# Optimization experiments

Measured on AMD Instinct MI355X. Metric: run time of the kernel, lower is better.

The kernel has to match this reference:

```python
import jax, jax.numpy as jnp
import numpy as np

N, E, NG = 4096, 8192, 256
AF, BF, H, L = 9, 4, 128, 3
LN_EPS = 1e-5


def _layernorm(x, g, b):
    mu = jnp.mean(x, axis=-1, keepdims=True)
    var = jnp.var(x, axis=-1, keepdims=True)
    return (x - mu) * jax.lax.rsqrt(var + LN_EPS) * g + b


def setup_inputs() -> dict:
    key = jax.random.key(0)
    ks = jax.random.split(key, 20)
    x = jax.random.normal(ks[0], (N, AF), dtype=jnp.float32)
    edge_index = jax.random.randint(ks[1], (2, E), 0, N, dtype=jnp.int64)
    edge_attr = jax.random.normal(ks[2], (E, BF), dtype=jnp.float32)
    batch = jnp.sort(jax.random.randint(ks[3], (N,), 0, NG, dtype=jnp.int64))
    s = lambda f: 1.0 / np.sqrt(f)
    return {
        "x": x, "edge_index": edge_index, "edge_attr": edge_attr, "batch": batch,
        "atom_w": jax.random.normal(ks[4], (AF, H), jnp.float32) * s(AF),
        "atom_b": jnp.zeros((H,), jnp.float32),
        # per-layer edge-network params, stacked over L layers
        "e1_w": jax.random.normal(ks[5], (L, BF, H), jnp.float32) * s(BF),
        "e1_b": jnp.zeros((L, H), jnp.float32),
        "e2_w": jax.random.normal(ks[6], (L, H, H * H), jnp.float32) * s(H),
        "e2_b": jnp.zeros((L, H * H), jnp.float32),
        "root_w": jax.random.normal(ks[7], (L, H, H), jnp.float32) * s(H),
        "conv_b": jnp.zeros((L, H), jnp.float32),
        "ln_g": jnp.ones((L, H), jnp.float32),
        "ln_b": jnp.zeros((L, H), jnp.float32),
        "head_w1": jax.random.normal(ks[8], (H, H // 2), jnp.float32) * s(H),
        "head_b1": jnp.zeros((H // 2,), jnp.float32),
        "head_w2": jax.random.normal(ks[9], (H // 2, 1), jnp.float32) * s(H // 2),
        "head_b2": jnp.zeros((1,), jnp.float32),
    }


def reference(x, edge_index, edge_attr, batch, atom_w, atom_b, e1_w, e1_b,
              e2_w, e2_b, root_w, conv_b, ln_g, ln_b, head_w1, head_b1,
              head_w2, head_b2):
    src, dst = edge_index[0], edge_index[1]
    h = jax.nn.relu(x @ atom_w + atom_b)  # [N, H]
    # in-degree for mean aggregation (empty -> 0 via clamp on denominator)
    deg = jax.ops.segment_sum(jnp.ones((E,), h.dtype), dst, num_segments=N)
    denom = jnp.maximum(deg, 1.0)[:, None]
    for l in range(L):
        # edge network: bond features -> per-edge HxH weight matrix
        eh = jax.nn.gelu(edge_attr @ e1_w[l] + e1_b[l], approximate=False)
        w = (eh @ e2_w[l] + e2_b[l]).reshape(E, H, H)  # [E, H, H]
        # gather source node features, per-edge matvec, scatter-mean to dst
        msg = jnp.einsum('ei,eio->eo', h[src], w)  # [E, H]
        agg = jax.ops.segment_sum(msg, dst, num_segments=N) / denom
        h_new = jax.nn.relu(agg + h @ root_w[l] + conv_b[l])
        h = _layernorm(h + h_new, ln_g[l], ln_b[l])
        # dropout: eval mode (identity)
    # global mean pool over graphs
    cnt = jnp.maximum(jax.ops.segment_sum(jnp.ones((N,), h.dtype), batch, num_segments=NG), 1.0)
    mol = jax.ops.segment_sum(h, batch, num_segments=NG) / cnt[:, None]
    hid = jax.nn.gelu(mol @ head_w1 + head_b1, approximate=False)
    logits = (hid @ head_w2 + head_b2).squeeze(-1)  # [NG]
    return logits
```

## Files before the change

### kernel.cpp

```cpp
#include <hip/hip_runtime.h>
#include <hip/hip_bf16.h>

#define N_NODES 4096
#define N_EDGES 8192
#define NGRAPH  256
#define AFEAT   9
#define BFEAT   4
#define H       128
#define NL      3
#define KS      129
#define SPLITS  4
#define TILE_E  64
#define NPB     4
#define SLICE_SH    16384
#define SLICE_BYTES 32768

#define EMLP_BLOCKS (H * (N_EDGES / 256))
#define ATOM_BLOCKS (N_NODES / 2)
#define PREP_BLOCKS (NL * KS * 4)

typedef short short8 __attribute__((ext_vector_type(8)));
typedef float f32x4 __attribute__((ext_vector_type(4)));

__device__ __forceinline__ short f2b(float f){
    union { float f; unsigned u; } c; c.f = f;
    unsigned r = c.u + 0x7FFFu + ((c.u >> 16) & 1u);
    return (short)(r >> 16);
}
__device__ __forceinline__ float gelu_exact(float x){
    return 0.5f * x * (1.0f + erff(x * 0.70710678118654752440f));
}

__global__ void k_fused_pre(const float* __restrict__ ea, const float* __restrict__ w1,
                            const float* __restrict__ b1, float* __restrict__ ehT,
                            const float* __restrict__ x, const float* __restrict__ aw,
                            const float* __restrict__ ab, float* __restrict__ h,
                            short* __restrict__ hb,
                            const float* __restrict__ e2w, const float* __restrict__ e2b,
                            short* __restrict__ bt){
    __shared__ float smem[H * 33];
    int bid = blockIdx.x, tid = threadIdx.x;

    if (bid < EMLP_BLOCKS){
        int o = bid >> 5;
        int e = (bid & 31) * 256 + tid;
        float4 a = *(const float4*)(ea + (size_t)e * BFEAT);
        #pragma unroll
        for (int l = 0; l < NL; ++l){
            float v = b1[l * H + o]
                    + a.x * w1[(l * BFEAT + 0) * H + o]
                    + a.y * w1[(l * BFEAT + 1) * H + o]
                    + a.z * w1[(l * BFEAT + 2) * H + o]
                    + a.w * w1[(l * BFEAT + 3) * H + o];
            v = gelu_exact(v);
            ehT[((size_t)l * KS + o) * N_EDGES + e] = v;
            if (o == 0) ehT[((size_t)l * KS + H) * N_EDGES + e] = 1.0f;
        }
    } else if (bid < EMLP_BLOCKS + ATOM_BLOCKS){
        int b = bid - EMLP_BLOCKS;
        int half = tid >> 7, o = tid & 127;
        int n = b * 2 + half;
        float* xs = smem + half * 16;
        if (o < AFEAT) xs[o] = x[n * AFEAT + o];
        __syncthreads();
        float a = ab[o];
        #pragma unroll
        for (int f = 0; f < AFEAT; ++f) a += xs[f] * aw[f * H + o];
        a = fmaxf(a, 0.0f);
        h[(size_t)n * H + o]  = a;
        hb[(size_t)n * H + o] = f2b(a);
    } else {
        int b  = bid - (EMLP_BLOCKS + ATOM_BLOCKS);
        int o0 = (b & 3) * 32;
        int k  = (b >> 2) % KS;
        int l  = (b >> 2) / KS;
        const float* src = (k < H) ? (e2w + ((size_t)l * H + k) * (H * H))
                                   : (e2b + (size_t)l * (H * H));
        for (int idx = tid; idx < H * 32; idx += 256){
            int i = idx >> 5, op = idx & 31;
            smem[i * 33 + op] = src[i * H + o0 + op];
        }
        __syncthreads();
        short* dst = bt + (size_t)(l * KS + k) * SLICE_SH;
        for (int idx = tid; idx < 32 * H; idx += 256){
            int j    = idx & 7;
            int quad = (idx >> 3) & 3;
            int op   = (idx >> 5) & 31;
            int ic   = idx >> 10;
            int i    = ic * 32 + quad * 8 + j;
            int o    = o0 + op;
            dst[((((o >> 4) * 4 + ic) * 64) + quad * 16 + (o & 15)) * 8 + j]
                = f2b(smem[i * 33 + op]);
        }
    }
}

__global__ void k_csr(const int* __restrict__ ei, int* __restrict__ row_ptr,
                      int* __restrict__ eidx, float* __restrict__ molsum,
                      float* __restrict__ cnt){
    __shared__ int hist[N_NODES];
    __shared__ int part[256];
    int t = threadIdx.x;
    for (int i = t; i < N_NODES; i += 256) hist[i] = 0;
    for (int i = t; i < NGRAPH * H; i += 256) molsum[i] = 0.0f;
    for (int i = t; i < NGRAPH; i += 256) cnt[i] = 0.0f;
    __syncthreads();
    for (int e = t; e < N_EDGES; e += 256) atomicAdd(&hist[ei[N_EDGES + e]], 1);
    __syncthreads();
    int base = t * 16;
    int loc[16]; int s = 0;
    #pragma unroll
    for (int i = 0; i < 16; ++i){ loc[i] = s; s += hist[base + i]; }
    part[t] = s;
    __syncthreads();
    if (t == 0){
        int run = 0;
        for (int i = 0; i < 256; ++i){ int v = part[i]; part[i] = run; run += v; }
        row_ptr[N_NODES] = run;
    }
    __syncthreads();
    int off = part[t];
    #pragma unroll
    for (int i = 0; i < 16; ++i) row_ptr[base + i] = off + loc[i];
    __syncthreads();
    #pragma unroll
    for (int i = 0; i < 16; ++i) hist[base + i] = off + loc[i];
    __syncthreads();
    for (int e = t; e < N_EDGES; e += 256){
        int d = ei[N_EDGES + e];
        int pos = atomicAdd(&hist[d], 1);
        eidx[pos] = e;
    }
}

__global__ __launch_bounds__(256, 2)
void k_msg_gemm(const short* __restrict__ bt, const float* __restrict__ ehT,
                const short* __restrict__ hb, const int* __restrict__ ei,
                float* __restrict__ parts, int l){
    __shared__ __align__(16) float ehs[33 * TILE_E];

    const int tid  = threadIdx.x;
    const int lane = tid & 63, w = tid >> 6;
    const int col  = lane & 15, quad = lane >> 4;

    const int so    = blockIdx.x & 7;
    const int split = so & 3;
    const int ohalf = so >> 2;
    const int tile  = blockIdx.x >> 3;
    const int t     = ohalf * 4 + w;
    const int kbeg  = (KS * split) >> 2;
    const int kend  = (KS * (split + 1)) >> 2;
    const int kcnt  = kend - kbeg;
    const int ebase = tile * TILE_E;

    for (int idx = tid; idx < kcnt * TILE_E; idx += 256){
        int kk = idx >> 6, e = idx & 63;
        ehs[idx] = ehT[((size_t)(l * KS + kbeg + kk)) * N_EDGES + ebase + e];
    }

    short8 gf[4][4];
    #pragma unroll
    for (int m = 0; m < 4; ++m){
        int e = ebase + m * 16 + col;
        int s = ei[e];
        const char* gb = (const char*)hb + ((size_t)s * H + quad * 8) * 2;
        #pragma unroll
        for (int ic = 0; ic < 4; ++ic)
            gf[m][ic] = *(const short8*)(gb + ic * 64);
    }

    float acc[4][4];
    #pragma unroll
    for (int m = 0; m < 4; ++m)
        #pragma unroll
        for (int r = 0; r < 4; ++r) acc[m][r] = 0.0f;

    const char* bsrc = (const char*)bt + (size_t)(l * KS + kbeg) * SLICE_BYTES
                     + t * 4096 + lane * 16;

    short8 X[4], Y[4], Z[4];

    auto loadB = [&](short8 (&B)[4], int kk){
        const char* p = bsrc + (size_t)kk * SLICE_BYTES;
        #pragma unroll
        for (int ic = 0; ic < 4; ++ic)
            B[ic] = *(const short8*)(p + ic * 1024);
    };
    auto computeB = [&](const short8 (&B)[4], int kk){
        __builtin_amdgcn_s_setprio(1);
        #pragma unroll
        for (int m = 0; m < 4; ++m){
            f32x4 ev = *(const f32x4*)(ehs + kk * TILE_E + m * 16 + quad * 4);
            f32x4 U = {0.0f, 0.0f, 0.0f, 0.0f};
            #pragma unroll
            for (int ic = 0; ic < 4; ++ic)
                U = __builtin_amdgcn_mfma_f32_16x16x32_bf16(gf[m][ic], B[ic], U, 0, 0, 0);
            #pragma unroll
            for (int r = 0; r < 4; ++r)
                acc[m][r] += ev[r] * U[r];
        }
        __builtin_amdgcn_s_setprio(0);
    };

    loadB(X, 0); loadB(Y, 1); loadB(Z, 2);
    __syncthreads();

    int kk = 0;
    for (; kk + 3 < kcnt; kk += 3){
        computeB(X, kk);     loadB(X, kk + 3);
        computeB(Y, kk + 1); if (kk + 4 < kcnt) loadB(Y, kk + 4);
        computeB(Z, kk + 2); if (kk + 5 < kcnt) loadB(Z, kk + 5);
    }
    computeB(X, kk);
    if (kk + 1 < kcnt) computeB(Y, kk + 1);
    if (kk + 2 < kcnt) computeB(Z, kk + 2);

    float* pb = parts + ((size_t)ebase * SPLITS + split) * H + t * 16;
    #pragma unroll
    for (int m = 0; m < 4; ++m)
        #pragma unroll
        for (int r = 0; r < 4; ++r){
            int row = m * 16 + quad * 4 + r;
            pb[(size_t)row * SPLITS * H + col] = acc[m][r];
        }
}

__global__ void k_node(const float* __restrict__ parts, const int* __restrict__ eidx,
                       const int* __restrict__ row_ptr,
                       const float* __restrict__ rw, const float* __restrict__ cb,
                       const float* __restrict__ lg, const float* __restrict__ lb,
                       float* __restrict__ h, short* __restrict__ hb,
                       const int* __restrict__ batch, float* __restrict__ molsum,
                       float* __restrict__ cnt, int l, int dolast){
    __shared__ float hs[NPB][H];
    __shared__ float red[NPB][2][2];
    int n0 = blockIdx.x * NPB, o = threadIdx.x;
    const float* W = rw + (size_t)l * H * H;

    float hv[NPB], root[NPB], a[NPB];
    #pragma unroll
    for (int m = 0; m < NPB; ++m){
        hv[m] = h[(size_t)(n0 + m) * H + o];
        hs[m][o] = hv[m];
        root[m] = cb[l * H + o];
    }
    __syncthreads();

    #pragma unroll
    for (int m = 0; m < NPB; ++m){
        int p0 = row_ptr[n0 + m], p1 = row_ptr[n0 + m + 1];
        float s = 0.0f;
        for (int p = p0; p < p1; ++p){
            const float* pr = parts + (size_t)eidx[p] * SPLITS * H + o;
            #pragma unroll
            for (int sp = 0; sp < SPLITS; ++sp) s += pr[sp * H];
        }
        int d = p1 - p0;
        a[m] = s / (float)(d > 0 ? d : 1);
    }

    #pragma unroll 8
    for (int i = 0; i < H; ++i){
        float wv = W[i * H + o];
        #pragma unroll
        for (int m = 0; m < NPB; ++m) root[m] += hs[m][i] * wv;
    }

    float v[NPB];
    #pragma unroll
    for (int m = 0; m < NPB; ++m){
        float hn = fmaxf(a[m] + root[m], 0.0f);
        v[m] = hv[m] + hn;
        float s = v[m], q = v[m] * v[m];
        #pragma unroll
        for (int off = 32; off > 0; off >>= 1){
            s += __shfl_down(s, off, 64);
            q += __shfl_down(q, off, 64);
        }
        if ((o & 63) == 0){ red[m][0][o >> 6] = s; red[m][1][o >> 6] = q; }
    }
    __syncthreads();
    #pragma unroll
    for (int m = 0; m < NPB; ++m){
        float S = red[m][0][0] + red[m][0][1];
        float Q = red[m][1][0] + red[m][1][1];
        float mean = S * (1.0f / H);
        float var  = Q * (1.0f / H) - mean * mean;
        float out  = (v[m] - mean) * rsqrtf(var + 1e-5f) * lg[l * H + o] + lb[l * H + o];
        int n = n0 + m;
        h[(size_t)n * H + o]  = out;
        hb[(size_t)n * H + o] = f2b(out);
        if (dolast){
            int b = batch[n];
            atomicAdd(&molsum[b * H + o], out);
            if (o == 0) atomicAdd(&cnt[b], 1.0f);
        }
    }
}

__global__ void k_head(const float* __restrict__ molsum, const float* __restrict__ cnt,
                       const float* __restrict__ w1, const float* __restrict__ b1,
                       const float* __restrict__ w2, const float* __restrict__ b2,
                       float* __restrict__ out){
    __shared__ float mol[H];
    int g = blockIdx.x, t = threadIdx.x;
    float c = fmaxf(cnt[g], 1.0f);
    mol[t]      = molsum[g * H + t] / c;
    mol[t + 64] = molsum[g * H + t + 64] / c;
    __syncthreads();
    float a = b1[t];
    #pragma unroll 8
    for (int i = 0; i < H; ++i) a += mol[i] * w1[i * 64 + t];
    float hid = gelu_exact(a);
    float p = hid * w2[t];
    #pragma unroll
    for (int off = 32; off > 0; off >>= 1) p += __shfl_down(p, off, 64);
    if (t == 0) out[g] = p + b2[0];
}

extern "C" void kernel_launch(void* const* d_in, const int* in_sizes, int n_in,
                              void* d_out, int out_size, void* d_ws, size_t ws_size,
                              hipStream_t stream){
    (void)in_sizes; (void)n_in; (void)out_size; (void)ws_size;
    const float* x     = (const float*)d_in[0];
    const int*   ei    = (const int*)  d_in[1];
    const float* ea    = (const float*)d_in[2];
    const int*   batch = (const int*)  d_in[3];
    const float* aw    = (const float*)d_in[4];
    const float* ab    = (const float*)d_in[5];
    const float* e1w   = (const float*)d_in[6];
    const float* e1b   = (const float*)d_in[7];
    const float* e2w   = (const float*)d_in[8];
    const float* e2b   = (const float*)d_in[9];
    const float* rw    = (const float*)d_in[10];
    const float* cb    = (const float*)d_in[11];
    const float* lg    = (const float*)d_in[12];
    const float* lb    = (const float*)d_in[13];
    const float* hw1   = (const float*)d_in[14];
    const float* hb1   = (const float*)d_in[15];
    const float* hw2   = (const float*)d_in[16];
    const float* hb2   = (const float*)d_in[17];
    float* out = (float*)d_out;

    char* p = (char*)d_ws;
    auto carve = [&](size_t bytes){ char* r = p; p += (bytes + 255) & ~(size_t)255; return r; };
    short* bt     = (short*)carve((size_t)NL * KS * SLICE_SH * 2);
    float* h      = (float*)carve((size_t)N_NODES * H * 4);
    short* hbuf   = (short*)carve((size_t)N_NODES * H * 2);
    float* ehT    = (float*)carve((size_t)NL * KS * N_EDGES * 4);
    float* parts  = (float*)carve((size_t)N_EDGES * SPLITS * H * 4);
    int*   row_ptr= (int*)  carve((size_t)(N_NODES + 1) * 4);
    int*   eidx   = (int*)  carve((size_t)N_EDGES * 4);
    float* molsum = (float*)carve((size_t)NGRAPH * H * 4);
    float* cnt    = (float*)carve((size_t)NGRAPH * 4);

    k_fused_pre<<<EMLP_BLOCKS + ATOM_BLOCKS + PREP_BLOCKS, 256, 0, stream>>>(
        ea, e1w, e1b, ehT, x, aw, ab, h, hbuf, e2w, e2b, bt);
    k_csr<<<1, 256, 0, stream>>>(ei, row_ptr, eidx, molsum, cnt);

    for (int l = 0; l < NL; ++l){
        k_msg_gemm<<<(N_EDGES / TILE_E) * 8, 256, 0, stream>>>(bt, ehT, hbuf, ei, parts, l);
        k_node<<<N_NODES / NPB, H, 0, stream>>>(parts, eidx, row_ptr, rw, cb, lg, lb,
                                                h, hbuf, batch, molsum, cnt, l,
                                                l == NL - 1 ? 1 : 0);
    }
    k_head<<<NGRAPH, 64, 0, stream>>>(molsum, cnt, hw1, hb1, hw2, hb2, out);
}
```

Before: 299.1 us.

## Fuse per-layer message GEMM and node update into one cooperative persistent kernel

Replaces the six per-layer launches (message GEMM plus node update for each of three layers) with a single cooperative kernel of 512 blocks. Each block handles two GEMM tiles and then eight nodes, with grid-wide syncs between phases. This removes launch gaps and per-kernel tails. In exchange it pays grid.sync costs, halves the GEMM block count (each block now loops over two units), and drops the setprio hints. A non-cooperative fallback path is kept.

```diff
diff --git a/kernel.cpp b/kernel.cpp
--- a/kernel.cpp
+++ b/kernel.cpp
@@ -1,5 +1,8 @@
 #include <hip/hip_runtime.h>
 #include <hip/hip_bf16.h>
+#include <hip/hip_cooperative_groups.h>
+
+namespace cg = cooperative_groups;
 
 #define N_NODES 4096
 #define N_EDGES 8192
@@ -11,7 +14,6 @@
 #define KS      129
 #define SPLITS  4
 #define TILE_E  64
-#define NPB     4
 #define SLICE_SH    16384
 #define SLICE_BYTES 32768
 
@@ -133,26 +135,25 @@
     }
 }
 
-__global__ __launch_bounds__(256, 2)
-void k_msg_gemm(const short* __restrict__ bt, const float* __restrict__ ehT,
-                const short* __restrict__ hb, const int* __restrict__ ei,
-                float* __restrict__ parts, int l){
-    __shared__ __align__(16) float ehs[33 * TILE_E];
-
+__device__ __forceinline__ void gemm_unit(int unit, int l,
+        const short* __restrict__ bt, const float* __restrict__ ehT,
+        const short* __restrict__ hb, const int* __restrict__ ei,
+        float* __restrict__ parts, float* ehs){
     const int tid  = threadIdx.x;
     const int lane = tid & 63, w = tid >> 6;
     const int col  = lane & 15, quad = lane >> 4;
 
-    const int so    = blockIdx.x & 7;
+    const int so    = unit & 7;
     const int split = so & 3;
     const int ohalf = so >> 2;
-    const int tile  = blockIdx.x >> 3;
+    const int tile  = unit >> 3;
     const int t     = ohalf * 4 + w;
     const int kbeg  = (KS * split) >> 2;
     const int kend  = (KS * (split + 1)) >> 2;
     const int kcnt  = kend - kbeg;
     const int ebase = tile * TILE_E;
 
+    __syncthreads();
     for (int idx = tid; idx < kcnt * TILE_E; idx += 256){
         int kk = idx >> 6, e = idx & 63;
         ehs[idx] = ehT[((size_t)(l * KS + kbeg + kk)) * N_EDGES + ebase + e];
@@ -187,7 +188,6 @@
             B[ic] = *(const short8*)(p + ic * 1024);
     };
     auto computeB = [&](const short8 (&B)[4], int kk){
-        __builtin_amdgcn_s_setprio(1);
         #pragma unroll
         for (int m = 0; m < 4; ++m){
             f32x4 ev = *(const f32x4*)(ehs + kk * TILE_E + m * 16 + quad * 4);
@@ -199,7 +199,6 @@
             for (int r = 0; r < 4; ++r)
                 acc[m][r] += ev[r] * U[r];
         }
-        __builtin_amdgcn_s_setprio(0);
     };
 
     loadB(X, 0); loadB(Y, 1); loadB(Z, 2);
@@ -225,29 +224,31 @@
         }
 }
 
-__global__ void k_node(const float* __restrict__ parts, const int* __restrict__ eidx,
-                       const int* __restrict__ row_ptr,
-                       const float* __restrict__ rw, const float* __restrict__ cb,
-                       const float* __restrict__ lg, const float* __restrict__ lb,
-                       float* __restrict__ h, short* __restrict__ hb,
-                       const int* __restrict__ batch, float* __restrict__ molsum,
-                       float* __restrict__ cnt, int l, int dolast){
-    __shared__ float hs[NPB][H];
-    __shared__ float red[NPB][2][2];
-    int n0 = blockIdx.x * NPB, o = threadIdx.x;
+__device__ __forceinline__ void node_phase(int bid, int l, int dolast,
+        const float* __restrict__ parts, const int* __restrict__ eidx,
+        const int* __restrict__ row_ptr, const float* __restrict__ rw,
+        const float* __restrict__ cb, const float* __restrict__ lg,
+        const float* __restrict__ lb, float* __restrict__ h,
+        short* __restrict__ hb, const int* __restrict__ batch,
+        float* __restrict__ molsum, float* __restrict__ cnt, char* smem){
+    float (*hs)[H]     = (float (*)[H])smem;
+    float (*red)[2][2] = (float (*)[2][2])(smem + 8 * H * 4);
+    int tid = threadIdx.x;
+    int sub = tid >> 7, o = tid & 127;
+    int n0  = bid * 8 + sub * 4;
     const float* W = rw + (size_t)l * H * H;
 
-    float hv[NPB], root[NPB], a[NPB];
-    #pragma unroll
-    for (int m = 0; m < NPB; ++m){
+    float hv[4], root[4], a[4];
+    #pragma unroll
+    for (int m = 0; m < 4; ++m){
         hv[m] = h[(size_t)(n0 + m) * H + o];
-        hs[m][o] = hv[m];
+        hs[sub * 4 + m][o] = hv[m];
         root[m] = cb[l * H + o];
     }
     __syncthreads();
 
     #pragma unroll
-    for (int m = 0; m < NPB; ++m){
+    for (int m = 0; m < 4; ++m){
         int p0 = row_ptr[n0 + m], p1 = row_ptr[n0 + m + 1];
         float s = 0.0f;
         for (int p = p0; p < p1; ++p){
@@ -263,12 +264,12 @@
     for (int i = 0; i < H; ++i){
         float wv = W[i * H + o];
         #pragma unroll
-        for (int m = 0; m < NPB; ++m) root[m] += hs[m][i] * wv;
-    }
-
-    float v[NPB];
-    #pragma unroll
-    for (int m = 0; m < NPB; ++m){
+        for (int m = 0; m < 4; ++m) root[m] += hs[sub * 4 + m][i] * wv;
+    }
+
+    float v[4];
+    #pragma unroll
+    for (int m = 0; m < 4; ++m){
         float hn = fmaxf(a[m] + root[m], 0.0f);
         v[m] = hv[m] + hn;
         float s = v[m], q = v[m] * v[m];
@@ -277,25 +278,68 @@
             s += __shfl_down(s, off, 64);
             q += __shfl_down(q, off, 64);
         }
-        if ((o & 63) == 0){ red[m][0][o >> 6] = s; red[m][1][o >> 6] = q; }
-    }
-    __syncthreads();
-    #pragma unroll
-    for (int m = 0; m < NPB; ++m){
-        float S = red[m][0][0] + red[m][0][1];
-        float Q = red[m][1][0] + red[m][1][1];
+        if ((o & 63) == 0){ red[sub*4+m][0][o >> 6] = s; red[sub*4+m][1][o >> 6] = q; }
+    }
+    __syncthreads();
+    #pragma unroll
+    for (int m = 0; m < 4; ++m){
+        float S = red[sub*4+m][0][0] + red[sub*4+m][0][1];
+        float Q = red[sub*4+m][1][0] + red[sub*4+m][1][1];
         float mean = S * (1.0f / H);
         float var  = Q * (1.0f / H) - mean * mean;
-        float out  = (v[m] - mean) * rsqrtf(var + 1e-5f) * lg[l * H + o] + lb[l * H + o];
+        float outv = (v[m] - mean) * rsqrtf(var + 1e-5f) * lg[l * H + o] + lb[l * H + o];
         int n = n0 + m;
-        h[(size_t)n * H + o]  = out;
-        hb[(size_t)n * H + o] = f2b(out);
+        h[(size_t)n * H + o]  = outv;
+        hb[(size_t)n * H + o] = f2b(outv);
         if (dolast){
             int b = batch[n];
-            atomicAdd(&molsum[b * H + o], out);
+            atomicAdd(&molsum[b * H + o], outv);
             if (o == 0) atomicAdd(&cnt[b], 1.0f);
         }
     }
+}
+
+__global__ __launch_bounds__(256, 2)
+void k_layers(const short* __restrict__ bt, const float* __restrict__ ehT,
+              const int* __restrict__ ei, float* __restrict__ parts,
+              const int* __restrict__ eidx, const int* __restrict__ row_ptr,
+              const float* __restrict__ rw, const float* __restrict__ cb,
+              const float* __restrict__ lg, const float* __restrict__ lb,
+              float* __restrict__ h, short* __restrict__ hb,
+              const int* __restrict__ batch, float* __restrict__ molsum,
+              float* __restrict__ cnt){
+    __shared__ __align__(16) char smem[33 * TILE_E * 4];
+    cg::grid_group grid = cg::this_grid();
+    int bid = blockIdx.x;
+    for (int l = 0; l < NL; ++l){
+        gemm_unit(bid,       l, bt, ehT, hb, ei, parts, (float*)smem);
+        gemm_unit(bid + 512, l, bt, ehT, hb, ei, parts, (float*)smem);
+        __threadfence(); grid.sync(); __threadfence();
+        node_phase(bid, l, (l == NL - 1) ? 1 : 0, parts, eidx, row_ptr,
+                   rw, cb, lg, lb, h, hb, batch, molsum, cnt, smem);
+        if (l + 1 < NL){ __threadfence(); grid.sync(); __threadfence(); }
+    }
+}
+
+__global__ __launch_bounds__(256, 2)
+void k_gemm2(const short* __restrict__ bt, const float* __restrict__ ehT,
+             const short* __restrict__ hb, const int* __restrict__ ei,
+             float* __restrict__ parts, int l){
+    __shared__ __align__(16) float ehs[33 * TILE_E];
+    gemm_unit(blockIdx.x,       l, bt, ehT, hb, ei, parts, ehs);
+    gemm_unit(blockIdx.x + 512, l, bt, ehT, hb, ei, parts, ehs);
+}
+
+__global__ void k_node8(const float* __restrict__ parts, const int* __restrict__ eidx,
+                        const int* __restrict__ row_ptr, const float* __restrict__ rw,
+                        const float* __restrict__ cb, const float* __restrict__ lg,
+                        const float* __restrict__ lb, float* __restrict__ h,
+                        short* __restrict__ hb, const int* __restrict__ batch,
+                        float* __restrict__ molsum, float* __restrict__ cnt,
+                        int l, int dolast){
+    __shared__ __align__(16) char smem[8 * H * 4 + 128];
+    node_phase(blockIdx.x, l, dolast, parts, eidx, row_ptr, rw, cb, lg, lb,
+               h, hb, batch, molsum, cnt, smem);
 }
 
 __global__ void k_head(const float* __restrict__ molsum, const float* __restrict__ cnt,
@@ -358,11 +402,20 @@
         ea, e1w, e1b, ehT, x, aw, ab, h, hbuf, e2w, e2b, bt);
     k_csr<<<1, 256, 0, stream>>>(ei, row_ptr, eidx, molsum, cnt);
 
-    for (int l = 0; l < NL; ++l){
-        k_msg_gemm<<<(N_EDGES / TILE_E) * 8, 256, 0, stream>>>(bt, ehT, hbuf, ei, parts, l);
-        k_node<<<N_NODES / NPB, H, 0, stream>>>(parts, eidx, row_ptr, rw, cb, lg, lb,
-                                                h, hbuf, batch, molsum, cnt, l,
-                                                l == NL - 1 ? 1 : 0);
+    void* kargs[15] = {
+        (void*)&bt, (void*)&ehT, (void*)&ei, (void*)&parts, (void*)&eidx,
+        (void*)&row_ptr, (void*)&rw, (void*)&cb, (void*)&lg, (void*)&lb,
+        (void*)&h, (void*)&hbuf, (void*)&batch, (void*)&molsum, (void*)&cnt
+    };
+    hipError_t rc = hipLaunchCooperativeKernel((void*)k_layers, dim3(512), dim3(256),
+                                               kargs, 0, stream);
+    if (rc != hipSuccess){
+        for (int l = 0; l < NL; ++l){
+            k_gemm2<<<512, 256, 0, stream>>>(bt, ehT, hbuf, ei, parts, l);
+            k_node8<<<512, 256, 0, stream>>>(parts, eidx, row_ptr, rw, cb, lg, lb,
+                                             h, hbuf, batch, molsum, cnt, l,
+                                             l == NL - 1 ? 1 : 0);
+        }
     }
     k_head<<<NGRAPH, 64, 0, stream>>>(molsum, cnt, hw1, hb1, hw2, hb2, out);
 }
```

New measurement: 1.099 ms. +267.5%, slower.
